# Kernel tuning notes

Hardware: AMD Instinct MI355X
Metric: run time of the kernel (lower is better)

Reference implementation:

```python
import jax, jax.numpy as jnp
import numpy as np
from jax import lax

B, S, D, F = 2, 4096, 1024, 4096
LN_EPS = 1e-6

def _layer_norm(x, scale, bias):
    mu = jnp.mean(x, axis=-1, keepdims=True)
    var = jnp.mean(jnp.square(x - mu), axis=-1, keepdims=True)
    return (x - mu) * lax.rsqrt(var + LN_EPS) * scale + bias

def _gate_loop(q, k, v, a):
    # max-headed GateLoop: one head per channel, scalar complex state per channel
    # h_t = a_t * h_{t-1} + k_t * v_t ; y_t = q_t * h_t
    kv = (k * v).astype(jnp.complex64)
    def comb(e1, e2):
        a1, x1 = e1
        a2, x2 = e2
        return (a1 * a2, a2 * x1 + x2)
    _, h = lax.associative_scan(comb, (a, kv), axis=1)
    return q.astype(jnp.complex64) * h

def setup_inputs() -> dict:
    key = jax.random.key(0)
    ks = jax.random.split(key, 12)
    sd = 1.0 / np.sqrt(D)
    sf = 1.0 / np.sqrt(F)
    return {
        "x": jax.random.normal(ks[0], (B, S, D), jnp.float32),
        "Wq": jax.random.normal(ks[1], (D, D), jnp.float32) * sd,
        "Wk": jax.random.normal(ks[2], (D, D), jnp.float32) * sd,
        "Wv": jax.random.normal(ks[3], (D, D), jnp.float32) * sd,
        "Wa": jax.random.normal(ks[4], (D, 2 * D), jnp.float32) * sd,
        "Wg": jax.random.normal(ks[5], (D, D), jnp.float32) * sd,
        "Wo": jax.random.normal(ks[6], (D, D), jnp.float32) * sd,
        "ln1_scale": jnp.ones((D,), jnp.float32),
        "ln1_bias": jnp.zeros((D,), jnp.float32),
        "W1": jax.random.normal(ks[7], (D, F), jnp.float32) * sd,
        "b1": jax.random.normal(ks[8], (F,), jnp.float32) * 1e-6,
        "W2": jax.random.normal(ks[9], (F, D), jnp.float32) * sf,
        "b2": jax.random.normal(ks[10], (D,), jnp.float32) * 1e-6,
        "ln2_scale": jnp.ones((D,), jnp.float32),
        "ln2_bias": jnp.zeros((D,), jnp.float32),
    }

def reference(x, Wq, Wk, Wv, Wa, Wg, Wo, ln1_scale, ln1_bias, W1, b1, W2, b2, ln2_scale, ln2_bias):
    q = x @ Wq
    k = x @ Wk
    v = x @ Wv
    a = x @ Wa
    a_real, a_imag = jnp.split(a, 2, axis=-1)
    a_c = a_real + 1j * a_imag
    magnitude = jnp.abs(a_c)
    phase = jnp.angle(a_c)
    a_c = jax.nn.sigmoid(magnitude).astype(jnp.complex64) * jnp.exp(1j * phase)
    g = x.astype(jnp.complex64) @ Wg.astype(jnp.complex64)
    y = _gate_loop(q, k, v, a_c)
    y = y * (g * jax.nn.sigmoid(g))  # silu on complex g
    y = y @ Wo.astype(jnp.complex64)
    y = y.real
    # dropout deterministic (training=False)
    y = _layer_norm(y + x, ln1_scale, ln1_bias)
    h = jax.nn.gelu(y @ W1 + b1)
    out = h @ W2 + b2
    out = _layer_norm(out + y, ln2_scale, ln2_bias)
    return out
```

## Files before the change

### kernel.cpp

```cpp
#include <hip/hip_runtime.h>
#include <cstdint>

typedef unsigned short u16;
typedef unsigned int u32;

#define AS1 __attribute__((address_space(1)))
#define AS3 __attribute__((address_space(3)))

typedef _Float16 f16x8 __attribute__((ext_vector_type(8)));
typedef float f32x4 __attribute__((ext_vector_type(4)));

static constexpr int Bb = 2, Ss = 4096, Dd = 1024, Ff = 4096;
static constexpr int Mtok = Bb * Ss;
static constexpr int NCH = 128;
static constexpr int TCH = Ss / NCH;
static constexpr int PW = 6144;

__device__ __forceinline__ float h2f(u16 u) {
    union { u16 u; _Float16 h; } w; w.u = u; return (float)w.h;
}
__device__ __forceinline__ u16 f2h(float f) {
    union { _Float16 h; u16 u; } w; w.h = (_Float16)f; return w.u;
}

__device__ __forceinline__ void gload_lds16(const u16* g, u16* l) {
    __builtin_amdgcn_global_load_lds((const AS1 u32*)g, (AS3 u32*)l, 16, 0, 0);
}

__global__ __launch_bounds__(256) void cvt_f32_f16(const float* __restrict__ src,
                                                   u16* __restrict__ dst) {
    const long i = ((long)blockIdx.x * 256 + threadIdx.x) * 4;
    float4 f = *(const float4*)(src + i);
    ushort4 o;
    o.x = f2h(f.x); o.y = f2h(f.y); o.z = f2h(f.z); o.w = f2h(f.w);
    *(ushort4*)(dst + i) = o;
}

__global__ __launch_bounds__(1024) void transpose_f32_f16(const float* __restrict__ src,
                                                          u16* __restrict__ dst,
                                                          int K, int N) {
    __shared__ u16 t[32][33];
    const int tx = threadIdx.x, ty = threadIdx.y;
    const int n0 = blockIdx.x * 32, k0 = blockIdx.y * 32;
    t[ty][tx] = f2h(src[(long)(k0 + ty) * N + n0 + tx]);
    __syncthreads();
    dst[(long)(n0 + ty) * K + k0 + tx] = t[tx][ty];
}

template <int EPI>
__global__ __launch_bounds__(256, 2) void gemm_bt(const u16* __restrict__ A,
                                                  const u16* __restrict__ BT,
                                                  u16* __restrict__ C,
                                                  const float* __restrict__ bias,
                                                  int M, int N, int K,
                                                  int lda, int ldc) {
    __shared__ __align__(16) u16 sA[128 * 32];
    __shared__ __align__(16) u16 sB[128 * 32];
    const int tid = threadIdx.x;
    const int tm = blockIdx.y * 128;
    const int tn = blockIdx.x * 128;
    const int w = tid >> 6;
    const int lane = tid & 63;
    const int wm = (w >> 1) * 64;
    const int wn = (w & 1) * 64;
    const int q = lane >> 4;
    const int r16 = lane & 15;

    f32x4 acc[4][4];
#pragma unroll
    for (int i = 0; i < 4; i++)
#pragma unroll
        for (int j = 0; j < 4; j++) acc[i][j] = (f32x4){0.f, 0.f, 0.f, 0.f};

    const int s0 = tid, s1 = 256 + tid;
    const int row0 = s0 >> 2, kc0 = (s0 & 3) * 8;
    const int row1 = s1 >> 2, kc1 = (s1 & 3) * 8;
    const u16* Ar0 = A + (long)(tm + row0) * lda + kc0;
    const u16* Ar1 = A + (long)(tm + row1) * lda + kc1;
    const u16* Br0 = BT + (long)(tn + row0) * K + kc0;
    const u16* Br1 = BT + (long)(tn + row1) * K + kc1;

    const int kiters = K >> 5;
    for (int kt = 0; kt < kiters; ++kt) {
        const int ko = kt * 32;
        gload_lds16(Ar0 + ko, sA + s0 * 8);
        gload_lds16(Ar1 + ko, sA + s1 * 8);
        gload_lds16(Br0 + ko, sB + s0 * 8);
        gload_lds16(Br1 + ko, sB + s1 * 8);
        __syncthreads();
        f16x8 af[4], bfr[4];
#pragma unroll
        for (int mi = 0; mi < 4; mi++)
            af[mi] = *(const f16x8*)(sA + (wm + mi * 16 + r16) * 32 + q * 8);
#pragma unroll
        for (int ni = 0; ni < 4; ni++)
            bfr[ni] = *(const f16x8*)(sB + (wn + ni * 16 + r16) * 32 + q * 8);
#pragma unroll
        for (int mi = 0; mi < 4; mi++)
#pragma unroll
            for (int ni = 0; ni < 4; ni++)
                acc[mi][ni] = __builtin_amdgcn_mfma_f32_16x16x32_f16(
                    af[mi], bfr[ni], acc[mi][ni], 0, 0, 0);
        __syncthreads();
    }

#pragma unroll
    for (int mi = 0; mi < 4; mi++) {
#pragma unroll
        for (int ni = 0; ni < 4; ni++) {
            const int gcol = tn + wn + ni * 16 + r16;
            float bv = 0.f;
            if (EPI) bv = bias[gcol];
#pragma unroll
            for (int j = 0; j < 4; j++) {
                const int grow = tm + wm + mi * 16 + q * 4 + j;
                float v = acc[mi][ni][j];
                if (EPI) v += bv;
                if (EPI == 1) {
                    float t = tanhf(0.7978845608028654f * (v + 0.044715f * v * v * v));
                    v = 0.5f * v * (1.0f + t);
                }
                C[(long)grow * ldc + gcol] = f2h(v);
            }
        }
    }
}

__device__ __forceinline__ void a_transform(float ar, float ai, float& cr, float& ci) {
    float m = sqrtf(ar * ar + ai * ai);
    float sg = 1.f / (1.f + __expf(-m));
    float sc = sg / fmaxf(m, 1e-30f);
    cr = ar * sc;
    ci = ai * sc;
}

__global__ __launch_bounds__(1024) void scan1(const u16* __restrict__ pcat,
                                              float4* __restrict__ sum4) {
    const int b = blockIdx.y, c = blockIdx.x, d = threadIdx.x;
    float Arp = 1.f, Aip = 0.f, Xr = 0.f, Xi = 0.f;
    const long rowbase = (long)b * Ss + (long)c * TCH;
#pragma unroll 4
    for (int s = 0; s < TCH; ++s) {
        const long ro = (rowbase + s) * PW;
        float ar = h2f(pcat[ro + 3072 + d]);
        float ai = h2f(pcat[ro + 4096 + d]);
        float kk = h2f(pcat[ro + 1024 + d]);
        float vv = h2f(pcat[ro + 2048 + d]);
        float cr, ci;
        a_transform(ar, ai, cr, ci);
        float kv = kk * vv;
        float nXr = cr * Xr - ci * Xi + kv;
        float nXi = cr * Xi + ci * Xr;
        Xr = nXr; Xi = nXi;
        float nAr = cr * Arp - ci * Aip;
        float nAi = cr * Aip + ci * Arp;
        Arp = nAr; Aip = nAi;
    }
    sum4[((long)b * NCH + c) * 1024 + d] = make_float4(Arp, Aip, Xr, Xi);
}

__global__ __launch_bounds__(256) void scan2(const float4* __restrict__ sum4,
                                             float2* __restrict__ carry) {
    const int idx = blockIdx.x * 256 + threadIdx.x;
    const int b = idx >> 10, d = idx & 1023;
    float hr = 0.f, hi = 0.f;
    for (int cb = 0; cb < NCH / 8; ++cb) {
        float4 t[8];
#pragma unroll
        for (int j = 0; j < 8; j++)
            t[j] = sum4[((long)b * NCH + cb * 8 + j) * 1024 + d];
#pragma unroll
        for (int j = 0; j < 8; j++) {
            carry[((long)b * NCH + cb * 8 + j) * 1024 + d] = make_float2(hr, hi);
            float nr = t[j].x * hr - t[j].y * hi + t[j].z;
            float ni = t[j].x * hi + t[j].y * hr + t[j].w;
            hr = nr; hi = ni;
        }
    }
}

__global__ __launch_bounds__(1024) void scan3(u16* pcat,
                                              const float2* __restrict__ carry) {
    const int b = blockIdx.y, c = blockIdx.x, d = threadIdx.x;
    float2 h0 = carry[((long)b * NCH + c) * 1024 + d];
    float hr = h0.x, hi = h0.y;
    const long rowbase = (long)b * Ss + (long)c * TCH;
#pragma unroll 4
    for (int s = 0; s < TCH; ++s) {
        const long ro = (rowbase + s) * PW;
        float ar = h2f(pcat[ro + 3072 + d]);
        float ai = h2f(pcat[ro + 4096 + d]);
        float kk = h2f(pcat[ro + 1024 + d]);
        float vv = h2f(pcat[ro + 2048 + d]);
        float cr, ci;
        a_transform(ar, ai, cr, ci);
        float kv = kk * vv;
        float nhr = cr * hr - ci * hi + kv;
        float nhi = cr * hi + ci * hr;
        hr = nhr; hi = nhi;
        float gg = h2f(pcat[ro + 5120 + d]);
        float si = gg / (1.f + __expf(-gg));
        float yv = h2f(pcat[ro + d]) * hr * si;
        pcat[ro + d] = f2h(yv);
    }
}

template <int RESF32, int OUTF32>
__global__ __launch_bounds__(256) void ln_kernel(const u16* __restrict__ a, int sa,
                                                 const void* __restrict__ bres, int sres,
                                                 const float* __restrict__ scale,
                                                 const float* __restrict__ bias,
                                                 void* __restrict__ out, int sout) {
    const int row = blockIdx.x;
    const int tid = threadIdx.x;
    const long abase = (long)row * sa;
    const long rbase = (long)row * sres;
    const long obase = (long)row * sout;
    float v[4];
#pragma unroll
    for (int j = 0; j < 4; j++) {
        int d = tid * 4 + j;
        float rb = RESF32 ? ((const float*)bres)[rbase + d]
                          : h2f(((const u16*)bres)[rbase + d]);
        v[j] = h2f(a[abase + d]) + rb;
    }
    float s = v[0] + v[1] + v[2] + v[3];
    float s2 = v[0] * v[0] + v[1] * v[1] + v[2] * v[2] + v[3] * v[3];
#pragma unroll
    for (int off = 32; off; off >>= 1) {
        s += __shfl_down(s, off);
        s2 += __shfl_down(s2, off);
    }
    __shared__ float red[8];
    const int w = tid >> 6, lane = tid & 63;
    if (lane == 0) { red[w] = s; red[4 + w] = s2; }
    __syncthreads();
    if (tid == 0) {
        float ts = red[0] + red[1] + red[2] + red[3];
        float ts2 = red[4] + red[5] + red[6] + red[7];
        float mu = ts * (1.f / 1024.f);
        float var = ts2 * (1.f / 1024.f) - mu * mu;
        red[0] = mu;
        red[1] = rsqrtf(var + 1e-6f);
    }
    __syncthreads();
    const float mu = red[0], rs = red[1];
#pragma unroll
    for (int j = 0; j < 4; j++) {
        int d = tid * 4 + j;
        float y = (v[j] - mu) * rs * scale[d] + bias[d];
        if (OUTF32) ((float*)out)[obase + d] = y;
        else        ((u16*)out)[obase + d] = f2h(y);
    }
}

extern "C" void kernel_launch(void* const* d_in, const int* in_sizes, int n_in,
                              void* d_out, int out_size, void* d_ws, size_t ws_size,
                              hipStream_t stream) {
    const float* x    = (const float*)d_in[0];
    const float* Wq   = (const float*)d_in[1];
    const float* Wk   = (const float*)d_in[2];
    const float* Wv   = (const float*)d_in[3];
    const float* Wa   = (const float*)d_in[4];
    const float* Wg   = (const float*)d_in[5];
    const float* Wo   = (const float*)d_in[6];
    const float* ln1s = (const float*)d_in[7];
    const float* ln1b = (const float*)d_in[8];
    const float* W1   = (const float*)d_in[9];
    const float* b1   = (const float*)d_in[10];
    const float* W2   = (const float*)d_in[11];
    const float* b2   = (const float*)d_in[12];
    const float* ln2s = (const float*)d_in[13];
    const float* ln2b = (const float*)d_in[14];

    u16* ws    = (u16*)d_ws;
    u16* xb    = ws;
    u16* WTcat = xb + (8u << 20);
    u16* WTo   = WTcat + (6u << 20);
    u16* WT1   = WTo + (1u << 20);
    u16* WT2   = WT1 + (4u << 20);
    u16* pcat  = WT2 + (4u << 20);

    float4* sum4  = (float4*)WTcat;
    float2* carry = (float2*)(WTcat + (2u << 20));


    cvt_f32_f16<<<dim3(8192), dim3(256), 0, stream>>>(x, xb);

    const dim3 tb(32, 32);
    transpose_f32_f16<<<dim3(32, 32), tb, 0, stream>>>(Wq, WTcat, 1024, 1024);
    transpose_f32_f16<<<dim3(32, 32), tb, 0, stream>>>(Wk, WTcat + (1u << 20), 1024, 1024);
    transpose_f32_f16<<<dim3(32, 32), tb, 0, stream>>>(Wv, WTcat + (2u << 20), 1024, 1024);
    transpose_f32_f16<<<dim3(64, 32), tb, 0, stream>>>(Wa, WTcat + (3u << 20), 1024, 2048);
    transpose_f32_f16<<<dim3(32, 32), tb, 0, stream>>>(Wg, WTcat + (5u << 20), 1024, 1024);
    transpose_f32_f16<<<dim3(32, 32), tb, 0, stream>>>(Wo, WTo, 1024, 1024);
    transpose_f32_f16<<<dim3(128, 32), tb, 0, stream>>>(W1, WT1, 1024, 4096);
    transpose_f32_f16<<<dim3(32, 128), tb, 0, stream>>>(W2, WT2, 4096, 1024);

    const dim3 gblk(256);
    gemm_bt<0><<<dim3(48, 64), gblk, 0, stream>>>(xb, WTcat, pcat, nullptr,
                                                  Mtok, PW, 1024, 1024, PW);
    scan1<<<dim3(NCH, Bb), 1024, 0, stream>>>(pcat, sum4);
    scan2<<<dim3(8), 256, 0, stream>>>(sum4, carry);
    scan3<<<dim3(NCH, Bb), 1024, 0, stream>>>(pcat, carry);
    gemm_bt<0><<<dim3(8, 64), gblk, 0, stream>>>(pcat, WTo, pcat + 1024, nullptr,
                                                 Mtok, 1024, 1024, PW, PW);
    ln_kernel<1, 0><<<dim3(Mtok), gblk, 0, stream>>>(pcat + 1024, PW, x, 1024,
                                                     ln1s, ln1b, pcat, PW);
    gemm_bt<1><<<dim3(32, 64), gblk, 0, stream>>>(pcat, WT1, pcat + 2048, b1,
                                                  Mtok, Ff, 1024, PW, PW);
    gemm_bt<2><<<dim3(8, 64), gblk, 0, stream>>>(pcat + 2048, WT2, pcat + 1024, b2,
                                                 Mtok, 1024, Ff, PW, PW);
    ln_kernel<0, 1><<<dim3(Mtok), gblk, 0, stream>>>(pcat + 1024, PW, pcat, PW,
                                                     ln2s, ln2b, d_out, 1024);
}
```

Measured before the change: 636.0 us.

## Add 256x256 eight-wave pipelined GEMM for projection and FFN1 layers

Introduces a new GEMM kernel with 256x256 output tiles, 512 threads (8 waves), a 64-wide K step, and direct global-to-LDS loads into double-buffered, XOR-swizzled shared memory. Loads for the next tiles are interleaved with the MFMA phases using barriers, waitcnt and s_setprio, and blocks are remapped so neighbouring blocks share inputs in cache. It replaces the smaller-tile GEMM for the fused QKV/A/G projection and the FFN1+GELU layer, aiming at more data reuse per LDS load and better overlap of memory and compute. The cost is a large 128KB LDS footprint and heavy register use, which limit occupancy.

```diff
diff --git a/kernel.cpp b/kernel.cpp
--- a/kernel.cpp
+++ b/kernel.cpp
@@ -106,6 +106,142 @@
 
 #pragma unroll
     for (int mi = 0; mi < 4; mi++) {
+#pragma unroll
+        for (int ni = 0; ni < 4; ni++) {
+            const int gcol = tn + wn + ni * 16 + r16;
+            float bv = 0.f;
+            if (EPI) bv = bias[gcol];
+#pragma unroll
+            for (int j = 0; j < 4; j++) {
+                const int grow = tm + wm + mi * 16 + q * 4 + j;
+                float v = acc[mi][ni][j];
+                if (EPI) v += bv;
+                if (EPI == 1) {
+                    float t = tanhf(0.7978845608028654f * (v + 0.044715f * v * v * v));
+                    v = 0.5f * v * (1.0f + t);
+                }
+                C[(long)grow * ldc + gcol] = f2h(v);
+            }
+        }
+    }
+}
+
+template <int EPI>
+__global__ __launch_bounds__(512, 2) void gemm8p(const u16* __restrict__ A,
+                                                 const u16* __restrict__ BT,
+                                                 u16* __restrict__ C,
+                                                 const float* __restrict__ bias,
+                                                 int M, int N, int K,
+                                                 int lda, int ldc) {
+    extern __shared__ u16 lds[];
+    const int tid = threadIdx.x;
+
+    const int ntn = N >> 8;
+    int bid = blockIdx.x;
+    {
+        const int cpx = gridDim.x >> 3;
+        bid = (bid & 7) * cpx + (bid >> 3);
+    }
+    const int tm = (bid / ntn) << 8;
+    const int tn = (bid % ntn) << 8;
+
+    const int srow = tid >> 3;
+    const int scol = ((tid & 7) ^ (srow & 7)) << 3;
+    const u16* Abase = A + (long)(tm + srow) * lda + scol;
+    const u16* Bbase = BT + (long)(tn + srow) * (long)K + scol;
+    const long lda64 = (long)lda << 6;
+    const long ldb64 = (long)K << 6;
+
+    const int nt = K >> 6;
+
+    auto stA = [&](u16* bufbase, int h, int kt) {
+        u16* d = bufbase + h * 8192 + tid * 8;
+        const u16* g = Abase + (long)(h * 128) * lda + (kt << 6);
+        gload_lds16(g, d);
+        gload_lds16(g + lda64, d + 4096);
+    };
+    auto stB = [&](u16* bufbase, int h, int kt) {
+        u16* d = bufbase + 16384 + h * 8192 + tid * 8;
+        const u16* g = Bbase + (long)(h * 128) * (long)K + (kt << 6);
+        gload_lds16(g, d);
+        gload_lds16(g + ldb64, d + 4096);
+    };
+
+    const int wid = tid >> 6, lane = tid & 63;
+    const int r16 = lane & 15, q = lane >> 4;
+    const int wm = (wid >> 2) * 128;
+    const int wn = (wid & 3) * 64;
+    const int r7 = r16 & 7;
+    const int cx0 = (q ^ r7) << 3;
+    const int cx1 = ((4 | q) ^ r7) << 3;
+    const int aoff = (wm + r16) * 64;
+    const int boff = 16384 + (wn + r16) * 64;
+
+    f32x4 acc[8][4];
+#pragma unroll
+    for (int i = 0; i < 8; i++)
+#pragma unroll
+        for (int j = 0; j < 4; j++) acc[i][j] = (f32x4){0.f, 0.f, 0.f, 0.f};
+
+    {
+        const int t1 = nt > 1 ? 1 : 0;
+        stA(lds, 0, 0);
+        stA(lds, 1, 0);
+        stB(lds, 0, 0);
+        stB(lds, 1, 0);
+        stB(lds + 32768, 0, t1);
+        stB(lds + 32768, 1, t1);
+    }
+
+    for (int it = 0; it < nt; ++it) {
+        u16* sb = lds + ((it & 1) << 15);
+        u16* so = lds + (((it & 1) ^ 1) << 15);
+        const int tA = (it + 1 < nt) ? it + 1 : nt - 1;
+        const int tB = (it + 2 < nt) ? it + 2 : nt - 1;
+
+        asm volatile("s_waitcnt vmcnt(4)" ::: "memory");
+        __builtin_amdgcn_s_barrier();
+
+        f16x8 vb[4][2];
+#pragma unroll
+        for (int ni = 0; ni < 4; ni++) {
+            vb[ni][0] = *(const f16x8*)(sb + boff + ni * 1024 + cx0);
+            vb[ni][1] = *(const f16x8*)(sb + boff + ni * 1024 + cx1);
+        }
+
+#pragma unroll
+        for (int p = 0; p < 4; ++p) {
+            f16x8 pa[2][2];
+#pragma unroll
+            for (int m2 = 0; m2 < 2; m2++) {
+                pa[m2][0] = *(const f16x8*)(sb + aoff + (2 * p + m2) * 1024 + cx0);
+                pa[m2][1] = *(const f16x8*)(sb + aoff + (2 * p + m2) * 1024 + cx1);
+            }
+            if (p == 0)      stA(so, 0, tA);
+            else if (p == 1) stA(so, 1, tA);
+            else if (p == 2) stB(sb, 0, tB);
+            else             stB(sb, 1, tB);
+            __builtin_amdgcn_s_barrier();
+            asm volatile("s_waitcnt lgkmcnt(0)" ::: "memory");
+            __builtin_amdgcn_s_setprio(1);
+#pragma unroll
+            for (int m2 = 0; m2 < 2; m2++)
+#pragma unroll
+                for (int ni = 0; ni < 4; ni++) {
+                    acc[2 * p + m2][ni] = __builtin_amdgcn_mfma_f32_16x16x32_f16(
+                        pa[m2][0], vb[ni][0], acc[2 * p + m2][ni], 0, 0, 0);
+                    acc[2 * p + m2][ni] = __builtin_amdgcn_mfma_f32_16x16x32_f16(
+                        pa[m2][1], vb[ni][1], acc[2 * p + m2][ni], 0, 0, 0);
+                }
+            __builtin_amdgcn_s_setprio(0);
+            __builtin_amdgcn_s_barrier();
+        }
+    }
+
+    asm volatile("s_waitcnt vmcnt(0)" ::: "memory");
+
+#pragma unroll
+    for (int mi = 0; mi < 8; mi++) {
 #pragma unroll
         for (int ni = 0; ni < 4; ni++) {
             const int gcol = tn + wn + ni * 16 + r16;
@@ -284,6 +420,15 @@
     float4* sum4  = (float4*)WTcat;
     float2* carry = (float2*)(WTcat + (2u << 20));
 
+    static bool attr_done = false;
+    if (!attr_done) {
+        hipFuncSetAttribute(reinterpret_cast<const void*>(&gemm8p<0>),
+                            hipFuncAttributeMaxDynamicSharedMemorySize, 131072);
+        hipFuncSetAttribute(reinterpret_cast<const void*>(&gemm8p<1>),
+                            hipFuncAttributeMaxDynamicSharedMemorySize, 131072);
+        attr_done = true;
+    }
+
 
     cvt_f32_f16<<<dim3(8192), dim3(256), 0, stream>>>(x, xb);
 
@@ -298,8 +443,8 @@
     transpose_f32_f16<<<dim3(32, 128), tb, 0, stream>>>(W2, WT2, 4096, 1024);
 
     const dim3 gblk(256);
-    gemm_bt<0><<<dim3(48, 64), gblk, 0, stream>>>(xb, WTcat, pcat, nullptr,
-                                                  Mtok, PW, 1024, 1024, PW);
+    gemm8p<0><<<dim3(768), dim3(512), 131072, stream>>>(xb, WTcat, pcat, nullptr,
+                                                        Mtok, PW, 1024, 1024, PW);
     scan1<<<dim3(NCH, Bb), 1024, 0, stream>>>(pcat, sum4);
     scan2<<<dim3(8), 256, 0, stream>>>(sum4, carry);
     scan3<<<dim3(NCH, Bb), 1024, 0, stream>>>(pcat, carry);
@@ -307,8 +452,8 @@
                                                  Mtok, 1024, 1024, PW, PW);
     ln_kernel<1, 0><<<dim3(Mtok), gblk, 0, stream>>>(pcat + 1024, PW, x, 1024,
                                                      ln1s, ln1b, pcat, PW);
-    gemm_bt<1><<<dim3(32, 64), gblk, 0, stream>>>(pcat, WT1, pcat + 2048, b1,
-                                                  Mtok, Ff, 1024, PW, PW);
+    gemm8p<1><<<dim3(512), dim3(512), 131072, stream>>>(pcat, WT1, pcat + 2048, b1,
+                                                        Mtok, Ff, 1024, PW, PW);
     gemm_bt<2><<<dim3(8, 64), gblk, 0, stream>>>(pcat + 2048, WT2, pcat + 1024, b2,
                                                  Mtok, 1024, Ff, PW, PW);
     ln_kernel<0, 1><<<dim3(Mtok), gblk, 0, stream>>>(pcat + 1024, PW, pcat, PW,
```

Result: faster. 611.9 us (-3.8%).
